# Optimization experiments

Hardware: AMD Instinct MI355X
Metric: run time of the kernel (lower is better)

## Reference

```python
import jax, jax.numpy as jnp
import numpy as np

BN_EPS = 1e-5
K = 3  # number of nearest neighbors for interpolation


def _square_distance(src, dst):
    # src: [B,N,3], dst: [B,S,3] -> [B,N,S]
    d = -2.0 * jnp.einsum('bnc,bsc->bns', src, dst)
    d = d + jnp.sum(src * src, axis=-1)[:, :, None]
    d = d + jnp.sum(dst * dst, axis=-1)[:, None, :]
    return d


def _conv_bn_relu(x, w, b, gamma, beta):
    # x: [B,C,N], w: [O,C], b: [O]
    y = jnp.einsum('bcn,oc->bon', x, w) + b[None, :, None]
    mean = jnp.mean(y, axis=(0, 2), keepdims=True)
    var = jnp.var(y, axis=(0, 2), keepdims=True)
    y = (y - mean) * jax.lax.rsqrt(var + BN_EPS)
    y = y * gamma[None, :, None] + beta[None, :, None]
    return jax.nn.relu(y)


def setup_inputs() -> dict:
    key = jax.random.key(0)
    ks = jax.random.split(key, 12)
    B, N, S, D1, D2 = 8, 8192, 2048, 256, 256
    Cin = D1 + D2
    xyz1 = jax.random.normal(ks[0], (B, N, 3), dtype=jnp.float32)
    xyz2 = jax.random.normal(ks[1], (B, S, 3), dtype=jnp.float32)
    points1 = jax.random.normal(ks[2], (B, D1, N), dtype=jnp.float32)
    points2 = jax.random.normal(ks[3], (B, D2, S), dtype=jnp.float32)
    w1 = jax.random.normal(ks[4], (256, Cin), dtype=jnp.float32) * (1.0 / np.sqrt(Cin))
    b1 = jnp.zeros((256,), dtype=jnp.float32)
    g1 = jnp.ones((256,), dtype=jnp.float32)
    be1 = jnp.zeros((256,), dtype=jnp.float32)
    w2 = jax.random.normal(ks[5], (256, 256), dtype=jnp.float32) * (1.0 / np.sqrt(256))
    b2 = jnp.zeros((256,), dtype=jnp.float32)
    g2 = jnp.ones((256,), dtype=jnp.float32)
    be2 = jnp.zeros((256,), dtype=jnp.float32)
    return {"xyz1": xyz1, "xyz2": xyz2, "points1": points1, "points2": points2,
            "w1": w1, "b1": b1, "g1": g1, "be1": be1,
            "w2": w2, "b2": b2, "g2": g2, "be2": be2}


def reference(xyz1, xyz2, points1, points2, w1, b1, g1, be1, w2, b2, g2, be2):
    B, N, _ = xyz1.shape
    dists = _square_distance(xyz1, xyz2)              # [B,N,S]
    neg_d, idx = jax.lax.top_k(-dists, K)             # 3 smallest distances
    d3 = -neg_d                                       # [B,N,3]
    dist_recip = 1.0 / (d3 + 1e-8)
    weight = dist_recip / jnp.sum(dist_recip, axis=2, keepdims=True)  # [B,N,3]
    p2 = jnp.swapaxes(points2, 1, 2)                  # [B,S,D2]
    gathered = jax.vmap(lambda pts, ix: pts[ix])(p2, idx)  # [B,N,3,D2]
    interp = jnp.sum(gathered * weight[..., None], axis=2)  # [B,N,D2]
    new_points = jnp.concatenate([jnp.swapaxes(points1, 1, 2), interp], axis=-1)  # [B,N,D1+D2]
    x = jnp.swapaxes(new_points, 1, 2)                # [B,Cin,N]
    x = _conv_bn_relu(x, w1, b1, g1, be1)
    x = _conv_bn_relu(x, w2, b2, g2, be2)
    return x
```

## Files before the change

### kernel.cpp

```cpp
#include <hip/hip_runtime.h>
#include <hip/hip_bf16.h>
#include <float.h>

#define BB 8
#define NNq 8192
#define SSk 2048
#define CIN 512
#define OC 256
#define NR (BB * NNq)
#define NBX 512
#define KNN_HALF 1024

typedef __attribute__((ext_vector_type(8))) short bf16x8;
typedef __attribute__((ext_vector_type(8))) unsigned short ushort8;
typedef __attribute__((ext_vector_type(4))) float f32x4;
typedef __attribute__((ext_vector_type(2))) float f32x2;

__device__ __forceinline__ unsigned short f2bf(float f) {
  union { __hip_bfloat16 h; unsigned short u; } v;
  v.h = __float2bfloat16(f);
  return v.u;
}
__device__ __forceinline__ float bf2f(unsigned short u) {
  union { unsigned int i; float f; } x; x.i = ((unsigned int)u) << 16; return x.f;
}

__device__ __forceinline__ f32x2 pkdist(f32x2 xp, f32x2 yp, f32x2 zp, f32x2 pp2,
                                        f32x2 cxy, f32x2 czw) {
  f32x2 t, m;
  asm("v_pk_mul_f32 %0, %2, %6 op_sel:[0,0] op_sel_hi:[1,0]\n\t"
      "v_pk_mul_f32 %1, %3, %6 op_sel:[0,1] op_sel_hi:[1,1]\n\t"
      "v_pk_add_f32 %0, %0, %1\n\t"
      "v_pk_mul_f32 %1, %4, %7 op_sel:[0,0] op_sel_hi:[1,0]\n\t"
      "v_pk_add_f32 %0, %0, %1\n\t"
      "v_pk_add_f32 %0, %0, %5\n\t"
      "v_pk_add_f32 %0, %0, %7 op_sel:[0,1] op_sel_hi:[1,1]"
      : "=&v"(t), "=&v"(m)
      : "v"(xp), "v"(yp), "v"(zp), "v"(pp2), "v"(cxy), "v"(czw));
  return t;
}

__global__ void k_misc(const float* __restrict__ w1, const float* __restrict__ w2,
                       const float* __restrict__ xyz2,
                       __hip_bfloat16* __restrict__ wb1, __hip_bfloat16* __restrict__ wb2,
                       float4* __restrict__ hq) {
  int i = blockIdx.x * 256 + threadIdx.x;
  if (i < 131072) {
    wb1[i] = __float2bfloat16(w1[i]);
  } else if (i < 196608) {
    int j = i - 131072;
    wb2[j] = __float2bfloat16(w2[j]);
  } else {
    int p = i - 196608;
    float x = xyz2[p * 3 + 0], y = xyz2[p * 3 + 1], z = xyz2[p * 3 + 2];
    float qq = __fadd_rn(__fadd_rn(__fmul_rn(x, x), __fmul_rn(y, y)), __fmul_rn(z, z));
    hq[p] = make_float4(-2.f * x, -2.f * y, -2.f * z, qq);
  }
}

__global__ __launch_bounds__(512) void k_knn(const float* __restrict__ xyz1,
                                             const float4* __restrict__ hq,
                                             float* __restrict__ pe, int* __restrict__ pi) {
  __shared__ float4 lsh[1536];
  float* meP = (float*)lsh;
  int*   miP = (int*)lsh + 3072;
  int b = blockIdx.y, half = blockIdx.z;
  int t = threadIdx.x;
  int lane = t & 63, w = t >> 6;

  const float4* __restrict__ hsrc = hq + (long)b * SSk + half * KNN_HALF;
  lsh[t] = hsrc[t];
  lsh[t + 512] = hsrc[t + 512];

  long baseA = (long)b * NNq + blockIdx.x * 128 + lane;
  long baseB = baseA + 64;
  float xa = xyz1[baseA * 3 + 0], ya = xyz1[baseA * 3 + 1], za = xyz1[baseA * 3 + 2];
  float xb_ = xyz1[baseB * 3 + 0], yb_ = xyz1[baseB * 3 + 1], zb_ = xyz1[baseB * 3 + 2];
  float ppa = __fadd_rn(__fadd_rn(__fmul_rn(xa, xa), __fmul_rn(ya, ya)), __fmul_rn(za, za));
  float ppb = __fadd_rn(__fadd_rn(__fmul_rn(xb_, xb_), __fmul_rn(yb_, yb_)), __fmul_rn(zb_, zb_));
  f32x2 xp = {xa, xb_}, yp = {ya, yb_}, zp = {za, zb_}, pp2 = {ppa, ppb};
  __syncthreads();

  float e0a = FLT_MAX, e1a = FLT_MAX, e2a = FLT_MAX;
  float e0b = FLT_MAX, e1b = FLT_MAX, e2b = FLT_MAX;
  int i0a = 0, i1a = 0, i2a = 0, i0b = 0, i1b = 0, i2b = 0;
  const f32x4* __restrict__ qp = (const f32x4*)(lsh + w * 128);
#pragma unroll 8
  for (int ii = 0; ii < 128; ++ii) {
    f32x4 c = qp[ii];
    f32x2 cxy = c.xy, czw = c.zw;
    f32x2 d2 = pkdist(xp, yp, zp, pp2, cxy, czw);
    float da = d2.x, db = d2.y;
    {
      bool c0 = da < e0a, c1 = da < e1a, c2 = da < e2a;
      int ni2 = c1 ? i1a : (c2 ? ii : i2a);
      int ni1 = c0 ? i0a : (c1 ? ii : i1a);
      int ni0 = c0 ? ii : i0a;
      float ne2 = __builtin_amdgcn_fmed3f(da, e1a, e2a);
      float ne1 = __builtin_amdgcn_fmed3f(da, e0a, e1a);
      e0a = fminf(e0a, da);
      e1a = ne1; e2a = ne2; i0a = ni0; i1a = ni1; i2a = ni2;
    }
    {
      bool c0 = db < e0b, c1 = db < e1b, c2 = db < e2b;
      int ni2 = c1 ? i1b : (c2 ? ii : i2b);
      int ni1 = c0 ? i0b : (c1 ? ii : i1b);
      int ni0 = c0 ? ii : i0b;
      float ne2 = __builtin_amdgcn_fmed3f(db, e1b, e2b);
      float ne1 = __builtin_amdgcn_fmed3f(db, e0b, e1b);
      e0b = fminf(e0b, db);
      e1b = ne1; e2b = ne2; i0b = ni0; i1b = ni1; i2b = ni2;
    }
  }
  __syncthreads();
  int s0 = half * KNN_HALF + w * 128;
  meP[(w * 3 + 0) * 128 + lane] = e0a; meP[(w * 3 + 1) * 128 + lane] = e1a; meP[(w * 3 + 2) * 128 + lane] = e2a;
  meP[(w * 3 + 0) * 128 + 64 + lane] = e0b; meP[(w * 3 + 1) * 128 + 64 + lane] = e1b; meP[(w * 3 + 2) * 128 + 64 + lane] = e2b;
  miP[(w * 3 + 0) * 128 + lane] = i0a + s0; miP[(w * 3 + 1) * 128 + lane] = i1a + s0; miP[(w * 3 + 2) * 128 + lane] = i2a + s0;
  miP[(w * 3 + 0) * 128 + 64 + lane] = i0b + s0; miP[(w * 3 + 1) * 128 + 64 + lane] = i1b + s0; miP[(w * 3 + 2) * 128 + 64 + lane] = i2b + s0;
  __syncthreads();

  if (t < 128) {
    float e0 = meP[0 * 128 + t], e1 = meP[1 * 128 + t], e2 = meP[2 * 128 + t];
    int   g0 = miP[0 * 128 + t], g1 = miP[1 * 128 + t], g2 = miP[2 * 128 + t];
    for (int ww = 1; ww < 8; ++ww) {
#pragma unroll
      for (int k = 0; k < 3; ++k) {
        float d = meP[(ww * 3 + k) * 128 + t]; int s = miP[(ww * 3 + k) * 128 + t];
        if (d < e2) {
          if (d < e1) {
            e2 = e1; g2 = g1;
            if (d < e0) { e1 = e0; g1 = g0; e0 = d; g0 = s; }
            else        { e1 = d; g1 = s; }
          } else { e2 = d; g2 = s; }
        }
      }
    }
    long base = (long)b * NNq + blockIdx.x * 128 + t;
    long o = ((long)half * NR + base) * 3;
    pe[o + 0] = e0; pe[o + 1] = e1; pe[o + 2] = e2;
    pi[o + 0] = g0; pi[o + 1] = g1; pi[o + 2] = g2;
  }
}

__global__ void k_tr_p1(const float* __restrict__ p1, __hip_bfloat16* __restrict__ xb) {
  __shared__ float tile[32][33];
  int b = blockIdx.z, c0 = blockIdx.y * 32, n0 = blockIdx.x * 32;
  int tx = threadIdx.x & 31, ty = threadIdx.x >> 5;
#pragma unroll
  for (int r = 0; r < 32; r += 8)
    tile[ty + r][tx] = p1[((long)(b * 256 + c0 + ty + r)) * NNq + n0 + tx];
  __syncthreads();
#pragma unroll
  for (int r = 0; r < 32; r += 8)
    xb[((long)(b * NNq + n0 + ty + r)) * CIN + c0 + tx] = __float2bfloat16(tile[tx][ty + r]);
}

__global__ void k_tr_p2(const float* __restrict__ p2, float* __restrict__ p2t) {
  __shared__ float tile[32][33];
  int b = blockIdx.z, c0 = blockIdx.y * 32, s0 = blockIdx.x * 32;
  int tx = threadIdx.x & 31, ty = threadIdx.x >> 5;
#pragma unroll
  for (int r = 0; r < 32; r += 8)
    tile[ty + r][tx] = p2[((long)(b * 256 + c0 + ty + r)) * SSk + s0 + tx];
  __syncthreads();
#pragma unroll
  for (int r = 0; r < 32; r += 8)
    p2t[((long)(b * SSk + s0 + ty + r)) * 256 + c0 + tx] = tile[tx][ty + r];
}

__global__ void k_gather(const float* __restrict__ p2t, const float* __restrict__ pe,
                         const int* __restrict__ pi, __hip_bfloat16* __restrict__ xb) {
  int b = blockIdx.y;
  int wid = threadIdx.x >> 6, lane = threadIdx.x & 63;
  int n = blockIdx.x * 4 + wid;
  long t = (long)b * NNq + n;
  float e0 = pe[t * 3 + 0], e1 = pe[t * 3 + 1], e2 = pe[t * 3 + 2];
  int   g0 = pi[t * 3 + 0], g1 = pi[t * 3 + 1], g2 = pi[t * 3 + 2];
  long o1 = ((long)NR + t) * 3;
#pragma unroll
  for (int k = 0; k < 3; ++k) {
    float d = pe[o1 + k]; int s = pi[o1 + k];
    if (d < e2) {
      if (d < e1) {
        e2 = e1; g2 = g1;
        if (d < e0) { e1 = e0; g1 = g0; e0 = d; g0 = s; }
        else        { e1 = d; g1 = s; }
      } else { e2 = d; g2 = s; }
    }
  }
  float r0 = 1.f / (e0 + 1e-8f), r1 = 1.f / (e1 + 1e-8f), r2 = 1.f / (e2 + 1e-8f);
  float rs = r0 + r1 + r2;
  float w0 = r0 / rs, w1 = r1 / rs, w2 = r2 / rs;

  const float4* q0 = (const float4*)(p2t + ((long)(b * SSk + g0)) * 256);
  const float4* q1 = (const float4*)(p2t + ((long)(b * SSk + g1)) * 256);
  const float4* q2 = (const float4*)(p2t + ((long)(b * SSk + g2)) * 256);
  float4 a = q0[lane], c = q1[lane], d = q2[lane];
  float vx = w0 * a.x + w1 * c.x + w2 * d.x;
  float vy = w0 * a.y + w1 * c.y + w2 * d.y;
  float vz = w0 * a.z + w1 * c.z + w2 * d.z;
  float vw = w0 * a.w + w1 * c.w + w2 * d.w;
  ushort4 u;
  u.x = f2bf(vx); u.y = f2bf(vy); u.z = f2bf(vz); u.w = f2bf(vw);
  *(ushort4*)((unsigned short*)xb + t * CIN + 256 + lane * 4) = u;
}

template <int K>
__global__ __launch_bounds__(256) void k_gemm(const __hip_bfloat16* __restrict__ X,
                                              const __hip_bfloat16* __restrict__ W,
                                              unsigned short* __restrict__ Yb,
                                              float* __restrict__ part) {
  constexpr int BK = 32;
  __shared__ __hip_bfloat16 xT[128 * BK];
  __shared__ __hip_bfloat16 wT[128 * BK];
  __shared__ float sb[4][4][16], qb[4][4][16];
  const int id = blockIdx.x;
  const int super = id >> 4, slot = id & 15;
  const int bx = super * 8 + (slot & 7);
  const int r0 = bx * 128;
  const int c0 = (slot >> 3) * 128;
  const int tid = threadIdx.x;
  const int wid = tid >> 6, lane = tid & 63;
  const int wr = wid >> 1, wc = wid & 1;
  f32x4 acc[4][4] = {};

  for (int kt = 0; kt < K; kt += BK) {
#pragma unroll
    for (int jj = 0; jj < 2; ++jj) {
      int j = wid * 2 + jj;
      int row = j * 16 + (lane >> 2);
      const __hip_bfloat16* g = X + ((long)(r0 + row)) * K + kt + (lane & 3) * 8;
      __builtin_amdgcn_global_load_lds((const __attribute__((address_space(1))) void*)(const void*)g,
                                       (__attribute__((address_space(3))) void*)(void*)(xT + j * 512),
                                       16, 0, 0);
    }
#pragma unroll
    for (int jj = 0; jj < 2; ++jj) {
      int j = wid * 2 + jj;
      int row = j * 16 + (lane >> 2);
      const __hip_bfloat16* g = W + ((long)(c0 + row)) * K + kt + (lane & 3) * 8;
      __builtin_amdgcn_global_load_lds((const __attribute__((address_space(1))) void*)(const void*)g,
                                       (__attribute__((address_space(3))) void*)(void*)(wT + j * 512),
                                       16, 0, 0);
    }
    __syncthreads();

    bf16x8 af[4], bfr[4];
#pragma unroll
    for (int m = 0; m < 4; ++m) {
      int row = wr * 64 + m * 16 + (lane & 15);
      af[m] = *(const bf16x8*)(xT + row * BK + (lane >> 4) * 8);
    }
#pragma unroll
    for (int nn = 0; nn < 4; ++nn) {
      int row = wc * 64 + nn * 16 + (lane & 15);
      bfr[nn] = *(const bf16x8*)(wT + row * BK + (lane >> 4) * 8);
    }
#pragma unroll
    for (int m = 0; m < 4; ++m)
#pragma unroll
      for (int nn = 0; nn < 4; ++nn)
        acc[m][nn] = __builtin_amdgcn_mfma_f32_16x16x32_bf16(af[m], bfr[nn], acc[m][nn], 0, 0, 0);
    __syncthreads();
  }

#pragma unroll
  for (int m = 0; m < 4; ++m)
#pragma unroll
    for (int nn = 0; nn < 4; ++nn)
#pragma unroll
      for (int reg = 0; reg < 4; ++reg) {
        int r = r0 + wr * 64 + m * 16 + (lane >> 4) * 4 + reg;
        int c = c0 + wc * 64 + nn * 16 + (lane & 15);
        Yb[(long)r * OC + c] = f2bf(acc[m][nn][reg]);
      }

#pragma unroll
  for (int nn = 0; nn < 4; ++nn) {
    float s = 0.f, q = 0.f;
#pragma unroll
    for (int m = 0; m < 4; ++m)
#pragma unroll
      for (int reg = 0; reg < 4; ++reg) {
        float v = acc[m][nn][reg];
        s += v; q += v * v;
      }
    s += __shfl_xor(s, 16); s += __shfl_xor(s, 32);
    q += __shfl_xor(q, 16); q += __shfl_xor(q, 32);
    if (lane < 16) { sb[wid][nn][lane] = s; qb[wid][nn][lane] = q; }
  }
  __syncthreads();
  if (tid < 128) {
    int col = tid & 15, nn = (tid >> 4) & 3, wcc = (tid >> 6) & 1;
    float s = sb[wcc][nn][col] + sb[2 + wcc][nn][col];
    float q = qb[wcc][nn][col] + qb[2 + wcc][nn][col];
    int ch = c0 + wcc * 64 + nn * 16 + col;
    part[(long)ch * NBX + bx] = s;
    part[(long)(256 + ch) * NBX + bx] = q;
  }
}

__global__ void k_scalefix(const float* __restrict__ part, const float* __restrict__ g,
                           const float* __restrict__ be, float* __restrict__ st) {
  __shared__ float sred[8][33], qred[8][33];
  int ch_l = threadIdx.x >> 5, j = threadIdx.x & 31;
  int o = blockIdx.x * 8 + ch_l;
  const float4* ps = (const float4*)(part + (long)o * NBX + j * 16);
  const float4* pq = (const float4*)(part + (long)(256 + o) * NBX + j * 16);
  float s = 0.f, q = 0.f;
#pragma unroll
  for (int i = 0; i < 4; ++i) {
    float4 a = ps[i], bq = pq[i];
    s += (a.x + a.y) + (a.z + a.w);
    q += (bq.x + bq.y) + (bq.z + bq.w);
  }
  sred[ch_l][j] = s; qred[ch_l][j] = q;
  __syncthreads();
  if (threadIdx.x < 8) {
    int ch = threadIdx.x;
    float ss = 0.f, qq = 0.f;
#pragma unroll
    for (int i = 0; i < 32; ++i) { ss += sred[ch][i]; qq += qred[ch][i]; }
    int oo = blockIdx.x * 8 + ch;
    float mean = ss * (1.f / NR);
    float var = qq * (1.f / NR) - mean * mean;
    float sc = g[oo] * rsqrtf(var + 1e-5f);
    st[oo] = sc;
    st[OC + oo] = be[oo] - mean * sc;
  }
}

__global__ void k_bnrelu_bf16(const unsigned short* __restrict__ Y, const float* __restrict__ st,
                              unsigned short* __restrict__ Yb) {
  long i8 = (long)blockIdx.x * 256 + threadIdx.x;
  ushort8 v = ((const ushort8*)Y)[i8];
  int c8 = (int)(i8 & 31);
  float4 sca = ((const float4*)st)[c8 * 2];
  float4 scb = ((const float4*)st)[c8 * 2 + 1];
  float4 sha = ((const float4*)(st + OC))[c8 * 2];
  float4 shb = ((const float4*)(st + OC))[c8 * 2 + 1];
  ushort8 u;
  u[0] = f2bf(fmaxf(fmaf(bf2f(v[0]), sca.x, sha.x), 0.f));
  u[1] = f2bf(fmaxf(fmaf(bf2f(v[1]), sca.y, sha.y), 0.f));
  u[2] = f2bf(fmaxf(fmaf(bf2f(v[2]), sca.z, sha.z), 0.f));
  u[3] = f2bf(fmaxf(fmaf(bf2f(v[3]), sca.w, sha.w), 0.f));
  u[4] = f2bf(fmaxf(fmaf(bf2f(v[4]), scb.x, shb.x), 0.f));
  u[5] = f2bf(fmaxf(fmaf(bf2f(v[5]), scb.y, shb.y), 0.f));
  u[6] = f2bf(fmaxf(fmaf(bf2f(v[6]), scb.z, shb.z), 0.f));
  u[7] = f2bf(fmaxf(fmaf(bf2f(v[7]), scb.w, shb.w), 0.f));
  ((ushort8*)Yb)[i8] = u;
}

__global__ void k_final(const unsigned short* __restrict__ Y, const float* __restrict__ st,
                        float* __restrict__ out) {
  __shared__ float tile[256][33];
  int b = blockIdx.z, o0 = blockIdx.y * 32, n0 = blockIdx.x * 256;
  int t = threadIdx.x;
  int cp = t & 15, tn = t >> 4;
  int c = cp * 2;
  float sc0 = st[o0 + c], sc1 = st[o0 + c + 1];
  float sh0 = st[OC + o0 + c], sh1 = st[OC + o0 + c + 1];
#pragma unroll
  for (int r = 0; r < 16; ++r) {
    int nl = r * 16 + tn;
    ushort2 v = *(const ushort2*)(Y + ((long)(b * NNq + n0 + nl)) * OC + o0 + c);
    tile[nl][c]     = fmaxf(fmaf(bf2f(v.x), sc0, sh0), 0.f);
    tile[nl][c + 1] = fmaxf(fmaf(bf2f(v.y), sc1, sh1), 0.f);
  }
  __syncthreads();
  int w = t >> 6, lane = t & 63;
#pragma unroll
  for (int rr = 0; rr < 8; ++rr) {
    int cl = w * 8 + rr;
    float4 v = make_float4(tile[lane * 4 + 0][cl], tile[lane * 4 + 1][cl],
                           tile[lane * 4 + 2][cl], tile[lane * 4 + 3][cl]);
    *(float4*)(out + ((long)(b * 256 + o0 + cl)) * NNq + n0 + lane * 4) = v;
  }
}

extern "C" void kernel_launch(void* const* d_in, const int* in_sizes, int n_in,
                              void* d_out, int out_size, void* d_ws, size_t ws_size,
                              hipStream_t stream) {
  const float* xyz1 = (const float*)d_in[0];
  const float* xyz2 = (const float*)d_in[1];
  const float* p1   = (const float*)d_in[2];
  const float* p2   = (const float*)d_in[3];
  const float* w1   = (const float*)d_in[4];
  const float* g1   = (const float*)d_in[6];
  const float* be1  = (const float*)d_in[7];
  const float* w2   = (const float*)d_in[8];
  const float* g2   = (const float*)d_in[10];
  const float* be2  = (const float*)d_in[11];
  float* out = (float*)d_out;

  char* ws = (char*)d_ws;
  const size_t OFF_XB   = 0;
  const size_t OFF_Y1   = 67108864;
  const size_t OFF_P2T  = OFF_Y1;
  const size_t OFF_PE   = OFF_Y1 + 16777216;
  const size_t OFF_PI   = OFF_PE + 1572864;
  const size_t OFF_MISC = 134217728;
  const size_t OFF_HQ   = OFF_MISC + 0;
  const size_t OFF_WB1  = OFF_MISC + 1835008;
  const size_t OFF_WB2  = OFF_MISC + 2097152;
  const size_t OFF_ST1  = OFF_MISC + 2228224;
  const size_t OFF_ST2  = OFF_MISC + 2230272;
  const size_t OFF_PART = OFF_MISC + 262144;

  __hip_bfloat16* xb   = (__hip_bfloat16*)(ws + OFF_XB);
  unsigned short* y1   = (unsigned short*)(ws + OFF_Y1);
  unsigned short* y2   = (unsigned short*)(ws + OFF_Y1);
  float* p2t           = (float*)(ws + OFF_P2T);
  float* pe            = (float*)(ws + OFF_PE);
  int*   pi            = (int*)(ws + OFF_PI);
  float4* hq           = (float4*)(ws + OFF_HQ);
  __hip_bfloat16* wb1  = (__hip_bfloat16*)(ws + OFF_WB1);
  __hip_bfloat16* wb2  = (__hip_bfloat16*)(ws + OFF_WB2);
  unsigned short* y1b  = (unsigned short*)(ws + OFF_XB);
  float* st1           = (float*)(ws + OFF_ST1);
  float* st2           = (float*)(ws + OFF_ST2);
  float* part          = (float*)(ws + OFF_PART);

  k_misc<<<832, 256, 0, stream>>>(w1, w2, xyz2, wb1, wb2, hq);
  k_knn<<<dim3(NNq / 128, BB, 2), 512, 0, stream>>>(xyz1, hq, pe, pi);
  k_tr_p1<<<dim3(NNq / 32, 256 / 32, BB), 256, 0, stream>>>(p1, xb);
  k_tr_p2<<<dim3(SSk / 32, 256 / 32, BB), 256, 0, stream>>>(p2, p2t);
  k_gather<<<dim3(NNq / 4, BB), 256, 0, stream>>>(p2t, pe, pi, xb);

  k_gemm<512><<<2 * NBX, 256, 0, stream>>>(xb, wb1, y1, part);
  k_scalefix<<<32, 256, 0, stream>>>(part, g1, be1, st1);
  k_bnrelu_bf16<<<(int)((long)NR * 256 / 8 / 256), 256, 0, stream>>>(y1, st1, y1b);

  k_gemm<256><<<2 * NBX, 256, 0, stream>>>((const __hip_bfloat16*)y1b, wb2, y2, part);
  k_scalefix<<<32, 256, 0, stream>>>(part, g2, be2, st2);
  k_final<<<dim3(NNq / 256, 256 / 32, BB), 256, 0, stream>>>(y2, st2, out);

  (void)in_sizes; (void)n_in; (void)out_size; (void)ws_size;
}
```

Measured before the change: 202.2 us.

## Merge KNN, transposes and weight conversion into one heterogeneous front kernel

Four front-end kernels (weight/xyz2 precompute, KNN, points1 transpose, points2 transpose) become one launch whose blocks pick a role from their block index. KNN blocks are interleaved with transpose blocks so the ALU-bound distance search overlaps with the memory-bound transposes. The xyz2 preprocessing moves into each KNN block, which removes the hq buffer and a dependency but recomputes it per block. The top-3 insertion is rewritten in inline asm with cndmask/med3 to shorten the inner loop. The cost is larger blocks, 512 threads with 24 KB of shared memory for every role, which may reduce occupancy for the transpose blocks.

```diff
diff --git a/kernel.cpp b/kernel.cpp
--- a/kernel.cpp
+++ b/kernel.cpp
@@ -40,133 +40,140 @@
   return t;
 }
 
-__global__ void k_misc(const float* __restrict__ w1, const float* __restrict__ w2,
-                       const float* __restrict__ xyz2,
-                       __hip_bfloat16* __restrict__ wb1, __hip_bfloat16* __restrict__ wb2,
-                       float4* __restrict__ hq) {
-  int i = blockIdx.x * 256 + threadIdx.x;
-  if (i < 131072) {
-    wb1[i] = __float2bfloat16(w1[i]);
-  } else if (i < 196608) {
-    int j = i - 131072;
-    wb2[j] = __float2bfloat16(w2[j]);
-  } else {
-    int p = i - 196608;
-    float x = xyz2[p * 3 + 0], y = xyz2[p * 3 + 1], z = xyz2[p * 3 + 2];
-    float qq = __fadd_rn(__fadd_rn(__fmul_rn(x, x), __fmul_rn(y, y)), __fmul_rn(z, z));
-    hq[p] = make_float4(-2.f * x, -2.f * y, -2.f * z, qq);
-  }
-}
-
-__global__ __launch_bounds__(512) void k_knn(const float* __restrict__ xyz1,
-                                             const float4* __restrict__ hq,
-                                             float* __restrict__ pe, int* __restrict__ pi) {
-  __shared__ float4 lsh[1536];
-  float* meP = (float*)lsh;
-  int*   miP = (int*)lsh + 3072;
-  int b = blockIdx.y, half = blockIdx.z;
-  int t = threadIdx.x;
-  int lane = t & 63, w = t >> 6;
-
-  const float4* __restrict__ hsrc = hq + (long)b * SSk + half * KNN_HALF;
-  lsh[t] = hsrc[t];
-  lsh[t + 512] = hsrc[t + 512];
-
-  long baseA = (long)b * NNq + blockIdx.x * 128 + lane;
-  long baseB = baseA + 64;
-  float xa = xyz1[baseA * 3 + 0], ya = xyz1[baseA * 3 + 1], za = xyz1[baseA * 3 + 2];
-  float xb_ = xyz1[baseB * 3 + 0], yb_ = xyz1[baseB * 3 + 1], zb_ = xyz1[baseB * 3 + 2];
-  float ppa = __fadd_rn(__fadd_rn(__fmul_rn(xa, xa), __fmul_rn(ya, ya)), __fmul_rn(za, za));
-  float ppb = __fadd_rn(__fadd_rn(__fmul_rn(xb_, xb_), __fmul_rn(yb_, yb_)), __fmul_rn(zb_, zb_));
-  f32x2 xp = {xa, xb_}, yp = {ya, yb_}, zp = {za, zb_}, pp2 = {ppa, ppb};
-  __syncthreads();
-
-  float e0a = FLT_MAX, e1a = FLT_MAX, e2a = FLT_MAX;
-  float e0b = FLT_MAX, e1b = FLT_MAX, e2b = FLT_MAX;
-  int i0a = 0, i1a = 0, i2a = 0, i0b = 0, i1b = 0, i2b = 0;
-  const f32x4* __restrict__ qp = (const f32x4*)(lsh + w * 128);
+__device__ __forceinline__ void insert3(float d, int ix, float& e0, float& e1, float& e2,
+                                        int& i0, int& i1, int& i2) {
+  int t;
+  asm("v_cmp_lt_f32 vcc, %[d], %[e2]\n\t"
+      "v_cndmask_b32 %[t], %[i2], %[ix], vcc\n\t"
+      "v_cmp_lt_f32 vcc, %[d], %[e1]\n\t"
+      "v_cndmask_b32 %[i2], %[t], %[i1], vcc\n\t"
+      "v_cndmask_b32 %[t], %[i1], %[ix], vcc\n\t"
+      "v_cmp_lt_f32 vcc, %[d], %[e0]\n\t"
+      "v_cndmask_b32 %[i1], %[t], %[i0], vcc\n\t"
+      "v_cndmask_b32 %[i0], %[i0], %[ix], vcc\n\t"
+      "v_med3_f32 %[e2], %[d], %[e1], %[e2]\n\t"
+      "v_med3_f32 %[e1], %[d], %[e0], %[e1]\n\t"
+      "v_min_f32 %[e0], %[e0], %[d]"
+      : [e0]"+v"(e0), [e1]"+v"(e1), [e2]"+v"(e2),
+        [i0]"+v"(i0), [i1]"+v"(i1), [i2]"+v"(i2), [t]"=&v"(t)
+      : [d]"v"(d), [ix]"v"(ix)
+      : "vcc");
+}
+
+__global__ __launch_bounds__(512) void k_front(const float* __restrict__ xyz1,
+                                               const float* __restrict__ xyz2,
+                                               const float* __restrict__ p1,
+                                               const float* __restrict__ p2,
+                                               const float* __restrict__ w1,
+                                               const float* __restrict__ w2,
+                                               float* __restrict__ pe, int* __restrict__ pi,
+                                               __hip_bfloat16* __restrict__ xb,
+                                               float* __restrict__ p2t,
+                                               __hip_bfloat16* __restrict__ wb1,
+                                               __hip_bfloat16* __restrict__ wb2) {
+  __shared__ char sm[24576];
+  int id = blockIdx.x;
+  int type, sub;
+  if (id < 2048)       { type = (id & 1) ? 1 : 0; sub = id >> 1; }
+  else if (id < 9216)  { type = 1; sub = 1024 + (id - 2048); }
+  else if (id < 11264) { type = 2; sub = id - 9216; }
+  else                 { type = 3; sub = id - 11264; }
+
+  if (type == 0) {
+    float4* lsh = (float4*)sm;
+    float* meP = (float*)sm;
+    int*   miP = (int*)sm + 3072;
+    int qblk = sub & 63, b = (sub >> 6) & 7, half = sub >> 9;
+    int t = threadIdx.x;
+    int lane = t & 63, w = t >> 6;
+
+#pragma unroll
+    for (int j = 0; j < 2; ++j) {
+      int p = t + j * 512;
+      const float* s = xyz2 + ((long)b * SSk + half * KNN_HALF + p) * 3;
+      float x = s[0], y = s[1], z = s[2];
+      float qq = __fadd_rn(__fadd_rn(__fmul_rn(x, x), __fmul_rn(y, y)), __fmul_rn(z, z));
+      lsh[p] = make_float4(-2.f * x, -2.f * y, -2.f * z, qq);
+    }
+
+    long baseA = (long)b * NNq + qblk * 128 + lane;
+    long baseB = baseA + 64;
+    float xa = xyz1[baseA * 3 + 0], ya = xyz1[baseA * 3 + 1], za = xyz1[baseA * 3 + 2];
+    float xb_ = xyz1[baseB * 3 + 0], yb_ = xyz1[baseB * 3 + 1], zb_ = xyz1[baseB * 3 + 2];
+    float ppa = __fadd_rn(__fadd_rn(__fmul_rn(xa, xa), __fmul_rn(ya, ya)), __fmul_rn(za, za));
+    float ppb = __fadd_rn(__fadd_rn(__fmul_rn(xb_, xb_), __fmul_rn(yb_, yb_)), __fmul_rn(zb_, zb_));
+    f32x2 xp = {xa, xb_}, yp = {ya, yb_}, zp = {za, zb_}, pp2 = {ppa, ppb};
+    __syncthreads();
+
+    float e0a = FLT_MAX, e1a = FLT_MAX, e2a = FLT_MAX;
+    float e0b = FLT_MAX, e1b = FLT_MAX, e2b = FLT_MAX;
+    int i0a = 0, i1a = 0, i2a = 0, i0b = 0, i1b = 0, i2b = 0;
+    const f32x4* __restrict__ qp = (const f32x4*)(lsh + w * 128);
 #pragma unroll 8
-  for (int ii = 0; ii < 128; ++ii) {
-    f32x4 c = qp[ii];
-    f32x2 cxy = c.xy, czw = c.zw;
-    f32x2 d2 = pkdist(xp, yp, zp, pp2, cxy, czw);
-    float da = d2.x, db = d2.y;
-    {
-      bool c0 = da < e0a, c1 = da < e1a, c2 = da < e2a;
-      int ni2 = c1 ? i1a : (c2 ? ii : i2a);
-      int ni1 = c0 ? i0a : (c1 ? ii : i1a);
-      int ni0 = c0 ? ii : i0a;
-      float ne2 = __builtin_amdgcn_fmed3f(da, e1a, e2a);
-      float ne1 = __builtin_amdgcn_fmed3f(da, e0a, e1a);
-      e0a = fminf(e0a, da);
-      e1a = ne1; e2a = ne2; i0a = ni0; i1a = ni1; i2a = ni2;
-    }
-    {
-      bool c0 = db < e0b, c1 = db < e1b, c2 = db < e2b;
-      int ni2 = c1 ? i1b : (c2 ? ii : i2b);
-      int ni1 = c0 ? i0b : (c1 ? ii : i1b);
-      int ni0 = c0 ? ii : i0b;
-      float ne2 = __builtin_amdgcn_fmed3f(db, e1b, e2b);
-      float ne1 = __builtin_amdgcn_fmed3f(db, e0b, e1b);
-      e0b = fminf(e0b, db);
-      e1b = ne1; e2b = ne2; i0b = ni0; i1b = ni1; i2b = ni2;
-    }
-  }
-  __syncthreads();
-  int s0 = half * KNN_HALF + w * 128;
-  meP[(w * 3 + 0) * 128 + lane] = e0a; meP[(w * 3 + 1) * 128 + lane] = e1a; meP[(w * 3 + 2) * 128 + lane] = e2a;
-  meP[(w * 3 + 0) * 128 + 64 + lane] = e0b; meP[(w * 3 + 1) * 128 + 64 + lane] = e1b; meP[(w * 3 + 2) * 128 + 64 + lane] = e2b;
-  miP[(w * 3 + 0) * 128 + lane] = i0a + s0; miP[(w * 3 + 1) * 128 + lane] = i1a + s0; miP[(w * 3 + 2) * 128 + lane] = i2a + s0;
-  miP[(w * 3 + 0) * 128 + 64 + lane] = i0b + s0; miP[(w * 3 + 1) * 128 + 64 + lane] = i1b + s0; miP[(w * 3 + 2) * 128 + 64 + lane] = i2b + s0;
-  __syncthreads();
-
-  if (t < 128) {
-    float e0 = meP[0 * 128 + t], e1 = meP[1 * 128 + t], e2 = meP[2 * 128 + t];
-    int   g0 = miP[0 * 128 + t], g1 = miP[1 * 128 + t], g2 = miP[2 * 128 + t];
-    for (int ww = 1; ww < 8; ++ww) {
-#pragma unroll
-      for (int k = 0; k < 3; ++k) {
-        float d = meP[(ww * 3 + k) * 128 + t]; int s = miP[(ww * 3 + k) * 128 + t];
-        if (d < e2) {
-          if (d < e1) {
-            e2 = e1; g2 = g1;
-            if (d < e0) { e1 = e0; g1 = g0; e0 = d; g0 = s; }
-            else        { e1 = d; g1 = s; }
-          } else { e2 = d; g2 = s; }
+    for (int ii = 0; ii < 128; ++ii) {
+      f32x4 c = qp[ii];
+      f32x2 d2 = pkdist(xp, yp, zp, pp2, c.xy, c.zw);
+      insert3(d2.x, ii, e0a, e1a, e2a, i0a, i1a, i2a);
+      insert3(d2.y, ii, e0b, e1b, e2b, i0b, i1b, i2b);
+    }
+    __syncthreads();
+    int s0 = half * KNN_HALF + w * 128;
+    meP[(w * 3 + 0) * 128 + lane] = e0a; meP[(w * 3 + 1) * 128 + lane] = e1a; meP[(w * 3 + 2) * 128 + lane] = e2a;
+    meP[(w * 3 + 0) * 128 + 64 + lane] = e0b; meP[(w * 3 + 1) * 128 + 64 + lane] = e1b; meP[(w * 3 + 2) * 128 + 64 + lane] = e2b;
+    miP[(w * 3 + 0) * 128 + lane] = i0a + s0; miP[(w * 3 + 1) * 128 + lane] = i1a + s0; miP[(w * 3 + 2) * 128 + lane] = i2a + s0;
+    miP[(w * 3 + 0) * 128 + 64 + lane] = i0b + s0; miP[(w * 3 + 1) * 128 + 64 + lane] = i1b + s0; miP[(w * 3 + 2) * 128 + 64 + lane] = i2b + s0;
+    __syncthreads();
+
+    if (t < 128) {
+      float e0 = meP[0 * 128 + t], e1 = meP[1 * 128 + t], e2 = meP[2 * 128 + t];
+      int   g0 = miP[0 * 128 + t], g1 = miP[1 * 128 + t], g2 = miP[2 * 128 + t];
+      for (int ww = 1; ww < 8; ++ww) {
+#pragma unroll
+        for (int k = 0; k < 3; ++k) {
+          float d = meP[(ww * 3 + k) * 128 + t]; int s = miP[(ww * 3 + k) * 128 + t];
+          if (d < e2) {
+            if (d < e1) {
+              e2 = e1; g2 = g1;
+              if (d < e0) { e1 = e0; g1 = g0; e0 = d; g0 = s; }
+              else        { e1 = d; g1 = s; }
+            } else { e2 = d; g2 = s; }
+          }
         }
       }
-    }
-    long base = (long)b * NNq + blockIdx.x * 128 + t;
-    long o = ((long)half * NR + base) * 3;
-    pe[o + 0] = e0; pe[o + 1] = e1; pe[o + 2] = e2;
-    pi[o + 0] = g0; pi[o + 1] = g1; pi[o + 2] = g2;
-  }
-}
-
-__global__ void k_tr_p1(const float* __restrict__ p1, __hip_bfloat16* __restrict__ xb) {
-  __shared__ float tile[32][33];
-  int b = blockIdx.z, c0 = blockIdx.y * 32, n0 = blockIdx.x * 32;
-  int tx = threadIdx.x & 31, ty = threadIdx.x >> 5;
-#pragma unroll
-  for (int r = 0; r < 32; r += 8)
-    tile[ty + r][tx] = p1[((long)(b * 256 + c0 + ty + r)) * NNq + n0 + tx];
-  __syncthreads();
-#pragma unroll
-  for (int r = 0; r < 32; r += 8)
-    xb[((long)(b * NNq + n0 + ty + r)) * CIN + c0 + tx] = __float2bfloat16(tile[tx][ty + r]);
-}
-
-__global__ void k_tr_p2(const float* __restrict__ p2, float* __restrict__ p2t) {
-  __shared__ float tile[32][33];
-  int b = blockIdx.z, c0 = blockIdx.y * 32, s0 = blockIdx.x * 32;
-  int tx = threadIdx.x & 31, ty = threadIdx.x >> 5;
-#pragma unroll
-  for (int r = 0; r < 32; r += 8)
-    tile[ty + r][tx] = p2[((long)(b * 256 + c0 + ty + r)) * SSk + s0 + tx];
-  __syncthreads();
-#pragma unroll
-  for (int r = 0; r < 32; r += 8)
-    p2t[((long)(b * SSk + s0 + ty + r)) * 256 + c0 + tx] = tile[tx][ty + r];
+      long base = (long)b * NNq + qblk * 128 + t;
+      long o = ((long)half * NR + base) * 3;
+      pe[o + 0] = e0; pe[o + 1] = e1; pe[o + 2] = e2;
+      pi[o + 0] = g0; pi[o + 1] = g1; pi[o + 2] = g2;
+    }
+  } else if (type == 1) {
+    int th = threadIdx.x & 255, hsub = threadIdx.x >> 8;
+    float (*T)[33] = (float(*)[33])((float*)sm + hsub * (32 * 33));
+    int b = sub >> 10, c0 = ((sub >> 7) & 7) * 32, n0 = (sub & 127) * 64 + hsub * 32;
+    int tx = th & 31, ty = th >> 5;
+#pragma unroll
+    for (int r = 0; r < 32; r += 8)
+      T[ty + r][tx] = p1[((long)(b * 256 + c0 + ty + r)) * NNq + n0 + tx];
+    __syncthreads();
+#pragma unroll
+    for (int r = 0; r < 32; r += 8)
+      xb[((long)(b * NNq + n0 + ty + r)) * CIN + c0 + tx] = __float2bfloat16(T[tx][ty + r]);
+  } else if (type == 2) {
+    int th = threadIdx.x & 255, hsub = threadIdx.x >> 8;
+    float (*T)[33] = (float(*)[33])((float*)sm + hsub * (32 * 33));
+    int b = sub >> 8, c0 = ((sub >> 5) & 7) * 32, s0 = (sub & 31) * 64 + hsub * 32;
+    int tx = th & 31, ty = th >> 5;
+#pragma unroll
+    for (int r = 0; r < 32; r += 8)
+      T[ty + r][tx] = p2[((long)(b * 256 + c0 + ty + r)) * SSk + s0 + tx];
+    __syncthreads();
+#pragma unroll
+    for (int r = 0; r < 32; r += 8)
+      p2t[((long)(b * SSk + s0 + ty + r)) * 256 + c0 + tx] = T[tx][ty + r];
+  } else {
+    int i = sub * 512 + threadIdx.x;
+    if (i < 131072) wb1[i] = __float2bfloat16(w1[i]);
+    else            wb2[i - 131072] = __float2bfloat16(w2[i - 131072]);
+  }
 }
 
 __global__ void k_gather(const float* __restrict__ p2t, const float* __restrict__ pe,
@@ -401,7 +408,6 @@
   const size_t OFF_PE   = OFF_Y1 + 16777216;
   const size_t OFF_PI   = OFF_PE + 1572864;
   const size_t OFF_MISC = 134217728;
-  const size_t OFF_HQ   = OFF_MISC + 0;
   const size_t OFF_WB1  = OFF_MISC + 1835008;
   const size_t OFF_WB2  = OFF_MISC + 2097152;
   const size_t OFF_ST1  = OFF_MISC + 2228224;
@@ -414,7 +420,6 @@
   float* p2t           = (float*)(ws + OFF_P2T);
   float* pe            = (float*)(ws + OFF_PE);
   int*   pi            = (int*)(ws + OFF_PI);
-  float4* hq           = (float4*)(ws + OFF_HQ);
   __hip_bfloat16* wb1  = (__hip_bfloat16*)(ws + OFF_WB1);
   __hip_bfloat16* wb2  = (__hip_bfloat16*)(ws + OFF_WB2);
   unsigned short* y1b  = (unsigned short*)(ws + OFF_XB);
@@ -422,10 +427,7 @@
   float* st2           = (float*)(ws + OFF_ST2);
   float* part          = (float*)(ws + OFF_PART);
 
-  k_misc<<<832, 256, 0, stream>>>(w1, w2, xyz2, wb1, wb2, hq);
-  k_knn<<<dim3(NNq / 128, BB, 2), 512, 0, stream>>>(xyz1, hq, pe, pi);
-  k_tr_p1<<<dim3(NNq / 32, 256 / 32, BB), 256, 0, stream>>>(p1, xb);
-  k_tr_p2<<<dim3(SSk / 32, 256 / 32, BB), 256, 0, stream>>>(p2, p2t);
+  k_front<<<11648, 512, 0, stream>>>(xyz1, xyz2, p1, p2, w1, w2, pe, pi, xb, p2t, wb1, wb2);
   k_gather<<<dim3(NNq / 4, BB), 256, 0, stream>>>(p2t, pe, pi, xb);
 
   k_gemm<512><<<2 * NBX, 256, 0, stream>>>(xb, wb1, y1, part);
```

Measured after the change: 228.8 us. 13.1% more time.
